# Performance work log

Hardware: AMD Instinct MI355X
Metric: run time of the kernel (lower is better)

## Reference

```python
import jax, jax.numpy as jnp
import numpy as np

N = 100000
E = 1200000


def _gcn_norm(edge_index, num_nodes):
    # Add self-loops and compute symmetric normalization (PyG GCNConv default).
    row = jnp.concatenate([edge_index[0], jnp.arange(num_nodes, dtype=edge_index.dtype)])
    col = jnp.concatenate([edge_index[1], jnp.arange(num_nodes, dtype=edge_index.dtype)])
    deg = jax.ops.segment_sum(jnp.ones_like(col, dtype=jnp.float32), col, num_segments=num_nodes)
    dinv = jnp.where(deg > 0, jax.lax.rsqrt(jnp.maximum(deg, 1.0)), 0.0)
    norm = dinv[row] * dinv[col]  # [E+N]
    return row, col, norm


def _gcn_conv(x, W, b, row, col, norm, num_nodes):
    h = x @ W                      # [N, out] dense transform first (fewer bytes to gather)
    msg = h[row] * norm[:, None]   # gather + edge-wise scale
    out = jax.ops.segment_sum(msg, col, num_segments=num_nodes)  # scatter-add to targets
    return out + b


def setup_inputs() -> dict:
    key = jax.random.key(0)
    k1, k2, k3, k4 = jax.random.split(key, 4)
    x = jax.random.normal(k1, (N, 128), dtype=jnp.float32)
    edge_index = jax.random.randint(k2, (2, E), 0, N, dtype=jnp.int64)
    W1 = jax.random.normal(k3, (128, 256), dtype=jnp.float32) * (1.0 / np.sqrt(128))
    b1 = jnp.zeros((256,), dtype=jnp.float32)
    W2 = jax.random.normal(k4, (256, 40), dtype=jnp.float32) * (1.0 / np.sqrt(256))
    b2 = jnp.zeros((40,), dtype=jnp.float32)
    return {"x": x, "edge_index": edge_index, "W1": W1, "b1": b1, "W2": W2, "b2": b2}


def reference(x, edge_index, W1, b1, W2, b2):
    row, col, norm = _gcn_norm(edge_index, N)
    h = _gcn_conv(x, W1, b1, row, col, norm, N)
    h = jax.nn.relu(h)
    # dropout omitted: eval mode (training=False) is identity
    return _gcn_conv(h, W2, b2, row, col, norm, N)
```

## Files before the change

### kernel.cpp

```cpp
#include <hip/hip_runtime.h>
#include <hip/hip_bf16.h>

#define NN 100000
#define EE 1200000
#define F1 128
#define F2 256
#define F3 40
#define MROWS 64
#define NBUK ((NN + 255) / 256)
#define NBLK 256
#define CHUNK ((EE + NBLK - 1) / NBLK)
#define DCAP 4096
#define XB2 ((NN * 32 + 255) / 256)
#define WB ((F1 * F2 + F2 * 48 + 255) / 256)

typedef __bf16 bf16x8 __attribute__((ext_vector_type(8)));
typedef float  f32x4  __attribute__((ext_vector_type(4)));

__device__ __forceinline__ unsigned short f2bf(float f) {
    unsigned u = __float_as_uint(f);
    return (unsigned short)((u + 0x7fffu + ((u >> 16) & 1u)) >> 16);
}
__device__ __forceinline__ float bflo(unsigned v) { return __uint_as_float(v << 16); }
__device__ __forceinline__ float bfhi(unsigned v) { return __uint_as_float(v & 0xffff0000u); }

__global__ __launch_bounds__(256) void k_scatprep(
    const int* __restrict__ row, const int* __restrict__ col,
    int* __restrict__ bcur, unsigned* __restrict__ rec,
    const float4* __restrict__ x, uint2* __restrict__ xh,
    const float* __restrict__ W1, const float* __restrict__ W2,
    __hip_bfloat16* __restrict__ W1p, __hip_bfloat16* __restrict__ W2p) {
    if (blockIdx.x < NBLK) {
        __shared__ int lh[NBUK];
        __shared__ int lbase[NBUK];
        for (int i = threadIdx.x; i < NBUK; i += 256) lh[i] = 0;
        __syncthreads();
        const int e0 = blockIdx.x * CHUNK;
        const int e1 = min(e0 + CHUNK, EE);
        for (int e = e0 + threadIdx.x; e < e1; e += 256) {
            int c = col[e];
            if ((unsigned)c < (unsigned)NN) atomicAdd(&lh[c >> 8], 1);
        }
        __syncthreads();
        for (int i = threadIdx.x; i < NBUK; i += 256) {
            int cn = lh[i];
            lbase[i] = cn ? atomicAdd(&bcur[i], cn) : 0;
            lh[i] = 0;
        }
        __syncthreads();
        for (int e = e0 + threadIdx.x; e < e1; e += 256) {
            int r = row[e], c = col[e];
            if ((unsigned)c < (unsigned)NN) {
                int b = c >> 8;
                int pos = lbase[b] + atomicAdd(&lh[b], 1);
                if (pos < DCAP)
                    rec[(size_t)b * DCAP + pos] =
                        ((unsigned)r & 0xFFFFFFu) | ((unsigned)(c & 255) << 24);
            }
        }
    } else if (blockIdx.x < NBLK + XB2) {
        int idx = (blockIdx.x - NBLK) * 256 + threadIdx.x;
        float4 v = x[idx];
        uint2 o;
        o.x = (unsigned)f2bf(v.x) | ((unsigned)f2bf(v.y) << 16);
        o.y = (unsigned)f2bf(v.z) | ((unsigned)f2bf(v.w) << 16);
        xh[idx] = o;
    } else {
        int idx = (blockIdx.x - NBLK - XB2) * 256 + threadIdx.x;
        if (idx < F1 * F2) {
            int k = idx / F2, c = idx - (idx / F2) * F2;
            int k8 = k >> 3, j = k & 7;
            W1p[((size_t)(k8 * F2 + c) << 3) + j] = __float2bfloat16(W1[(size_t)k * F2 + c]);
        } else {
            int i2 = idx - F1 * F2;
            int k = i2 / 48, c = i2 - (i2 / 48) * 48;
            int k8 = k >> 3, j = k & 7;
            float v = (c < F3) ? W2[(size_t)k * F3 + c] : 0.0f;
            W2p[((size_t)(k8 * 48 + c) << 3) + j] = __float2bfloat16(v);
        }
    }
}

__global__ __launch_bounds__(256) void k_csr(const int* __restrict__ bcur,
                                             const unsigned* __restrict__ rec,
                                             int* __restrict__ eidx,
                                             int* __restrict__ cnt,
                                             int* __restrict__ cursor,
                                             float* __restrict__ dinv) {
    __shared__ int lcnt[256];
    __shared__ int s[256];
    __shared__ int lcur[256];
    __shared__ unsigned lrec[DCAP];
    __shared__ int lde[DCAP];
    const int b = blockIdx.x;
    const int tid = threadIdx.x;
    lcnt[tid] = 0;
    __syncthreads();
    const int base = b * DCAP;
    const int nb = min(bcur[b], DCAP);
    for (int j = tid; j < nb; j += 256) {
        unsigned v = rec[(size_t)base + j];
        lrec[j] = v;
        atomicAdd(&lcnt[v >> 24], 1);
    }
    __syncthreads();
    int cv = lcnt[tid];
    s[tid] = cv;
    __syncthreads();
    int acc = cv;
    for (int d = 1; d < 256; d <<= 1) {
        int add = (tid >= d) ? s[tid - d] : 0;
        __syncthreads();
        acc += add;
        s[tid] = acc;
        __syncthreads();
    }
    int excl = acc - cv;
    lcur[tid] = excl;
    const int node = (b << 8) + tid;
    if (node < NN) {
        cnt[node] = cv;
        cursor[node] = base + excl + cv;
        dinv[node] = rsqrtf((float)(cv + 1));
    }
    __syncthreads();
    for (int j = tid; j < nb; j += 256) {
        unsigned v = lrec[j];
        int pos = atomicAdd(&lcur[v >> 24], 1);
        lde[pos] = (int)(v & 0xFFFFFFu);
    }
    __syncthreads();
    for (int j = tid; j < nb; j += 256) eidx[base + j] = lde[j];
}

__global__ __launch_bounds__(256) void k_agg1(const int* __restrict__ cursor,
                                              const int* __restrict__ cnt,
                                              const int* __restrict__ eidx,
                                              const float* __restrict__ dinv,
                                              const unsigned* __restrict__ xh,
                                              unsigned* __restrict__ agg) {
    int node = blockIdx.x * 4 + (threadIdx.x >> 6);
    int lane = threadIdx.x & 63;
    if (node >= NN) return;
    float dn = dinv[node];
    unsigned vs = xh[((size_t)node << 6) + lane];
    float a0 = bflo(vs) * dn, a1 = bfhi(vs) * dn;
    int n = cnt[node];
    int s = cursor[node] - n;
    int k = 0;
    for (; k + 7 < n; k += 8) {
        int r0 = eidx[s + k + 0], r1 = eidx[s + k + 1];
        int r2 = eidx[s + k + 2], r3 = eidx[s + k + 3];
        int r4 = eidx[s + k + 4], r5 = eidx[s + k + 5];
        int r6 = eidx[s + k + 6], r7 = eidx[s + k + 7];
        float d0 = dinv[r0], d1 = dinv[r1], d2 = dinv[r2], d3 = dinv[r3];
        float d4 = dinv[r4], d5 = dinv[r5], d6 = dinv[r6], d7 = dinv[r7];
        unsigned v0 = xh[((size_t)r0 << 6) + lane];
        unsigned v1 = xh[((size_t)r1 << 6) + lane];
        unsigned v2 = xh[((size_t)r2 << 6) + lane];
        unsigned v3 = xh[((size_t)r3 << 6) + lane];
        unsigned v4 = xh[((size_t)r4 << 6) + lane];
        unsigned v5 = xh[((size_t)r5 << 6) + lane];
        unsigned v6 = xh[((size_t)r6 << 6) + lane];
        unsigned v7 = xh[((size_t)r7 << 6) + lane];
        a0 += bflo(v0) * d0; a1 += bfhi(v0) * d0;
        a0 += bflo(v1) * d1; a1 += bfhi(v1) * d1;
        a0 += bflo(v2) * d2; a1 += bfhi(v2) * d2;
        a0 += bflo(v3) * d3; a1 += bfhi(v3) * d3;
        a0 += bflo(v4) * d4; a1 += bfhi(v4) * d4;
        a0 += bflo(v5) * d5; a1 += bfhi(v5) * d5;
        a0 += bflo(v6) * d6; a1 += bfhi(v6) * d6;
        a0 += bflo(v7) * d7; a1 += bfhi(v7) * d7;
    }
    for (; k + 3 < n; k += 4) {
        int r0 = eidx[s + k + 0], r1 = eidx[s + k + 1];
        int r2 = eidx[s + k + 2], r3 = eidx[s + k + 3];
        float d0 = dinv[r0], d1 = dinv[r1], d2 = dinv[r2], d3 = dinv[r3];
        unsigned v0 = xh[((size_t)r0 << 6) + lane];
        unsigned v1 = xh[((size_t)r1 << 6) + lane];
        unsigned v2 = xh[((size_t)r2 << 6) + lane];
        unsigned v3 = xh[((size_t)r3 << 6) + lane];
        a0 += bflo(v0) * d0; a1 += bfhi(v0) * d0;
        a0 += bflo(v1) * d1; a1 += bfhi(v1) * d1;
        a0 += bflo(v2) * d2; a1 += bfhi(v2) * d2;
        a0 += bflo(v3) * d3; a1 += bfhi(v3) * d3;
    }
    for (; k < n; ++k) {
        int r0 = eidx[s + k];
        float d0 = dinv[r0];
        unsigned v0 = xh[((size_t)r0 << 6) + lane];
        a0 += bflo(v0) * d0; a1 += bfhi(v0) * d0;
    }
    agg[((size_t)node << 6) + lane] = (unsigned)f2bf(a0 * dn) | ((unsigned)f2bf(a1 * dn) << 16);
}

__global__ __launch_bounds__(256) void k_gemm_mfma(
    const __hip_bfloat16* __restrict__ agg, const __hip_bfloat16* __restrict__ W1p,
    const float* __restrict__ b1, const __hip_bfloat16* __restrict__ W2p,
    const float* __restrict__ dinv, unsigned short* __restrict__ tg) {
    __shared__ __hip_bfloat16 h_s[MROWS][F2 + 8];
    const int i0   = blockIdx.x * MROWS;
    const int wave = threadIdx.x >> 6;
    const int lane = threadIdx.x & 63;
    const int m = lane & 15, q = lane >> 4;
    const int rowA = i0 + wave * 16 + m;

    f32x4 acc[16];
#pragma unroll
    for (int c = 0; c < 16; ++c) acc[c] = (f32x4){0.f, 0.f, 0.f, 0.f};

#pragma unroll
    for (int s = 0; s < 4; ++s) {
        bf16x8 a;
#pragma unroll
        for (int j = 0; j < 8; ++j) a[j] = (__bf16)0.0f;
        if (rowA < NN) a = *(const bf16x8*)(agg + (size_t)rowA * F1 + s * 32 + q * 8);
        const __hip_bfloat16* bp = W1p + ((size_t)(4 * s + q) * F2) * 8;
#pragma unroll
        for (int c = 0; c < 16; ++c) {
            bf16x8 b = *(const bf16x8*)(bp + ((size_t)(c * 16 + m) << 3));
            acc[c] = __builtin_amdgcn_mfma_f32_16x16x32_bf16(a, b, acc[c], 0, 0, 0);
        }
    }

#pragma unroll
    for (int c = 0; c < 16; ++c) {
        int col = c * 16 + m;
        float bj = b1[col];
#pragma unroll
        for (int r = 0; r < 4; ++r) {
            int lr = wave * 16 + q * 4 + r;
            h_s[lr][col] = __float2bfloat16(fmaxf(acc[c][r] + bj, 0.0f));
        }
    }
    __syncthreads();

    f32x4 acc2[3];
#pragma unroll
    for (int c = 0; c < 3; ++c) acc2[c] = (f32x4){0.f, 0.f, 0.f, 0.f};

#pragma unroll
    for (int s = 0; s < 8; ++s) {
        bf16x8 a = *(const bf16x8*)(&h_s[wave * 16 + m][s * 32 + q * 8]);
        const __hip_bfloat16* bp = W2p + ((size_t)(4 * s + q) * 48) * 8;
#pragma unroll
        for (int c = 0; c < 3; ++c) {
            bf16x8 b = *(const bf16x8*)(bp + ((size_t)(c * 16 + m) << 3));
            acc2[c] = __builtin_amdgcn_mfma_f32_16x16x32_bf16(a, b, acc2[c], 0, 0, 0);
        }
    }

#pragma unroll
    for (int c = 0; c < 3; ++c) {
        int col = c * 16 + m;
        if (col < F3) {
#pragma unroll
            for (int r = 0; r < 4; ++r) {
                int grow = i0 + wave * 16 + q * 4 + r;
                if (grow < NN)
                    tg[(size_t)grow * F3 + col] = f2bf(acc2[c][r] * dinv[grow]);
            }
        }
    }
}

__global__ __launch_bounds__(256) void k_agg2(const int* __restrict__ cursor,
                                              const int* __restrict__ cnt,
                                              const int* __restrict__ eidx,
                                              const float* __restrict__ dinv,
                                              const unsigned short* __restrict__ tg,
                                              const float* __restrict__ b2,
                                              float* __restrict__ out) {
    const int wave = threadIdx.x >> 6;
    const int lane = threadIdx.x & 63;
    const int g = lane / 10;
    const int t = lane - g * 10;
    const int node = blockIdx.x * 24 + wave * 6 + g;
    if (g >= 6 || node >= NN) return;
    const uint2* __restrict__ tg2 = (const uint2*)tg;

    uint2 v = tg2[(size_t)node * 10 + t];
    float a0 = bflo(v.x), a1 = bfhi(v.x), a2 = bflo(v.y), a3 = bfhi(v.y);
    const int n = cnt[node];
    const int s = cursor[node] - n;
    int k = 0;
    for (; k + 7 < n; k += 8) {
        int r0 = eidx[s + k + 0], r1 = eidx[s + k + 1];
        int r2 = eidx[s + k + 2], r3 = eidx[s + k + 3];
        int r4 = eidx[s + k + 4], r5 = eidx[s + k + 5];
        int r6 = eidx[s + k + 6], r7 = eidx[s + k + 7];
        uint2 v0 = tg2[(size_t)r0 * 10 + t];
        uint2 v1 = tg2[(size_t)r1 * 10 + t];
        uint2 v2 = tg2[(size_t)r2 * 10 + t];
        uint2 v3 = tg2[(size_t)r3 * 10 + t];
        uint2 v4 = tg2[(size_t)r4 * 10 + t];
        uint2 v5 = tg2[(size_t)r5 * 10 + t];
        uint2 v6 = tg2[(size_t)r6 * 10 + t];
        uint2 v7 = tg2[(size_t)r7 * 10 + t];
        a0 += bflo(v0.x); a1 += bfhi(v0.x); a2 += bflo(v0.y); a3 += bfhi(v0.y);
        a0 += bflo(v1.x); a1 += bfhi(v1.x); a2 += bflo(v1.y); a3 += bfhi(v1.y);
        a0 += bflo(v2.x); a1 += bfhi(v2.x); a2 += bflo(v2.y); a3 += bfhi(v2.y);
        a0 += bflo(v3.x); a1 += bfhi(v3.x); a2 += bflo(v3.y); a3 += bfhi(v3.y);
        a0 += bflo(v4.x); a1 += bfhi(v4.x); a2 += bflo(v4.y); a3 += bfhi(v4.y);
        a0 += bflo(v5.x); a1 += bfhi(v5.x); a2 += bflo(v5.y); a3 += bfhi(v5.y);
        a0 += bflo(v6.x); a1 += bfhi(v6.x); a2 += bflo(v6.y); a3 += bfhi(v6.y);
        a0 += bflo(v7.x); a1 += bfhi(v7.x); a2 += bflo(v7.y); a3 += bfhi(v7.y);
    }
    for (; k + 3 < n; k += 4) {
        int r0 = eidx[s + k + 0], r1 = eidx[s + k + 1];
        int r2 = eidx[s + k + 2], r3 = eidx[s + k + 3];
        uint2 v0 = tg2[(size_t)r0 * 10 + t];
        uint2 v1 = tg2[(size_t)r1 * 10 + t];
        uint2 v2 = tg2[(size_t)r2 * 10 + t];
        uint2 v3 = tg2[(size_t)r3 * 10 + t];
        a0 += bflo(v0.x); a1 += bfhi(v0.x); a2 += bflo(v0.y); a3 += bfhi(v0.y);
        a0 += bflo(v1.x); a1 += bfhi(v1.x); a2 += bflo(v1.y); a3 += bfhi(v1.y);
        a0 += bflo(v2.x); a1 += bfhi(v2.x); a2 += bflo(v2.y); a3 += bfhi(v2.y);
        a0 += bflo(v3.x); a1 += bfhi(v3.x); a2 += bflo(v3.y); a3 += bfhi(v3.y);
    }
    for (; k < n; ++k) {
        uint2 v0 = tg2[(size_t)eidx[s + k] * 10 + t];
        a0 += bflo(v0.x); a1 += bfhi(v0.x); a2 += bflo(v0.y); a3 += bfhi(v0.y);
    }
    float d = dinv[node];
    float4 bb = *(const float4*)(b2 + 4 * t);
    float4 o;
    o.x = a0 * d + bb.x;
    o.y = a1 * d + bb.y;
    o.z = a2 * d + bb.z;
    o.w = a3 * d + bb.w;
    *(float4*)(out + (size_t)node * F3 + 4 * t) = o;
}

extern "C" void kernel_launch(void* const* d_in, const int* in_sizes, int n_in,
                              void* d_out, int out_size, void* d_ws, size_t ws_size,
                              hipStream_t stream) {
    const float* x  = (const float*)d_in[0];
    const int*   ei = (const int*)d_in[1];
    const float* W1 = (const float*)d_in[2];
    const float* b1 = (const float*)d_in[3];
    const float* W2 = (const float*)d_in[4];
    const float* b2 = (const float*)d_in[5];
    float* out = (float*)d_out;

    const int* row = ei;
    const int* col = ei + EE;

    int* cnt     = (int*)d_ws;
    int* cursor  = cnt + NN;
    float* dinv  = (float*)(cursor + NN);
    int* bcur    = (int*)(dinv + NN);
    int* eidx    = bcur + NBUK + 9;
    unsigned* xh  = (unsigned*)(eidx + NBUK * DCAP);
    unsigned* agg = xh + (size_t)NN * 64;
    unsigned* rec = agg;
    unsigned short* tg = (unsigned short*)xh;
    __hip_bfloat16* W1p = (__hip_bfloat16*)(agg + (size_t)NN * 64);
    __hip_bfloat16* W2p = W1p + (size_t)F1 * F2;

    hipMemsetAsync(bcur, 0, NBUK * sizeof(int), stream);
    k_scatprep<<<NBLK + XB2 + WB, 256, 0, stream>>>(
        row, col, bcur, rec, (const float4*)x, (uint2*)xh, W1, W2, W1p, W2p);
    k_csr<<<NBUK, 256, 0, stream>>>(bcur, rec, eidx, cnt, cursor, dinv);

    k_agg1<<<(NN + 3) / 4, 256, 0, stream>>>(cursor, cnt, eidx, dinv, xh, agg);
    k_gemm_mfma<<<(NN + MROWS - 1) / MROWS, 256, 0, stream>>>(
        (const __hip_bfloat16*)agg, W1p, b1, W2p, dinv, tg);
    k_agg2<<<(NN + 23) / 24, 256, 0, stream>>>(cursor, cnt, eidx, dinv, tg, b2, out);
}
```

Baseline: 266.2 us.

## Slice bf16 features into 8 column planes so aggregation gathers stay cache-local

The bf16 copy of x is stored as 8 column slices of 16 features each (32 bytes per node per slice). Layer-1 aggregation then runs one block per (node group, slice), with 8 edges handled in parallel per wave and a shuffle reduction at the end. The GEMM reads its A operand from the same sliced layout. The aim is to keep each slice's gather working set (about 3.2 MB) small enough to hit in cache. The cost is 8x as many aggregation blocks, each reading eidx and dinv again, plus shorter 32-byte gather segments.

```diff
diff --git a/kernel.cpp b/kernel.cpp
--- a/kernel.cpp
+++ b/kernel.cpp
@@ -11,7 +11,7 @@
 #define NBLK 256
 #define CHUNK ((EE + NBLK - 1) / NBLK)
 #define DCAP 4096
-#define XB2 ((NN * 32 + 255) / 256)
+#define XP8 (NN * 8 / 256)
 #define WB ((F1 * F2 + F2 * 48 + 255) / 256)
 
 typedef __bf16 bf16x8 __attribute__((ext_vector_type(8)));
@@ -27,7 +27,7 @@
 __global__ __launch_bounds__(256) void k_scatprep(
     const int* __restrict__ row, const int* __restrict__ col,
     int* __restrict__ bcur, unsigned* __restrict__ rec,
-    const float4* __restrict__ x, uint2* __restrict__ xh,
+    const float4* __restrict__ x, unsigned* __restrict__ xhs,
     const float* __restrict__ W1, const float* __restrict__ W2,
     __hip_bfloat16* __restrict__ W1p, __hip_bfloat16* __restrict__ W2p) {
     if (blockIdx.x < NBLK) {
@@ -58,15 +58,24 @@
                         ((unsigned)r & 0xFFFFFFu) | ((unsigned)(c & 255) << 24);
             }
         }
-    } else if (blockIdx.x < NBLK + XB2) {
+    } else if (blockIdx.x < NBLK + XP8) {
         int idx = (blockIdx.x - NBLK) * 256 + threadIdx.x;
-        float4 v = x[idx];
-        uint2 o;
-        o.x = (unsigned)f2bf(v.x) | ((unsigned)f2bf(v.y) << 16);
-        o.y = (unsigned)f2bf(v.z) | ((unsigned)f2bf(v.w) << 16);
-        xh[idx] = o;
+        int node = idx >> 3, s = idx & 7;
+        const float4* xp = x + (size_t)node * 32 + s * 4;
+        float4 v0 = xp[0], v1 = xp[1], v2 = xp[2], v3 = xp[3];
+        uint4 o0, o1;
+        o0.x = (unsigned)f2bf(v0.x) | ((unsigned)f2bf(v0.y) << 16);
+        o0.y = (unsigned)f2bf(v0.z) | ((unsigned)f2bf(v0.w) << 16);
+        o0.z = (unsigned)f2bf(v1.x) | ((unsigned)f2bf(v1.y) << 16);
+        o0.w = (unsigned)f2bf(v1.z) | ((unsigned)f2bf(v1.w) << 16);
+        o1.x = (unsigned)f2bf(v2.x) | ((unsigned)f2bf(v2.y) << 16);
+        o1.y = (unsigned)f2bf(v2.z) | ((unsigned)f2bf(v2.w) << 16);
+        o1.z = (unsigned)f2bf(v3.x) | ((unsigned)f2bf(v3.y) << 16);
+        o1.w = (unsigned)f2bf(v3.z) | ((unsigned)f2bf(v3.w) << 16);
+        uint4* dst = (uint4*)(xhs + ((size_t)s * NN + node) * 8);
+        dst[0] = o0; dst[1] = o1;
     } else {
-        int idx = (blockIdx.x - NBLK - XB2) * 256 + threadIdx.x;
+        int idx = (blockIdx.x - NBLK - XP8) * 256 + threadIdx.x;
         if (idx < F1 * F2) {
             int k = idx / F2, c = idx - (idx / F2) * F2;
             int k8 = k >> 3, j = k & 7;
@@ -137,65 +146,51 @@
                                               const int* __restrict__ cnt,
                                               const int* __restrict__ eidx,
                                               const float* __restrict__ dinv,
-                                              const unsigned* __restrict__ xh,
-                                              unsigned* __restrict__ agg) {
-    int node = blockIdx.x * 4 + (threadIdx.x >> 6);
-    int lane = threadIdx.x & 63;
-    if (node >= NN) return;
-    float dn = dinv[node];
-    unsigned vs = xh[((size_t)node << 6) + lane];
-    float a0 = bflo(vs) * dn, a1 = bfhi(vs) * dn;
-    int n = cnt[node];
-    int s = cursor[node] - n;
-    int k = 0;
-    for (; k + 7 < n; k += 8) {
-        int r0 = eidx[s + k + 0], r1 = eidx[s + k + 1];
-        int r2 = eidx[s + k + 2], r3 = eidx[s + k + 3];
-        int r4 = eidx[s + k + 4], r5 = eidx[s + k + 5];
-        int r6 = eidx[s + k + 6], r7 = eidx[s + k + 7];
-        float d0 = dinv[r0], d1 = dinv[r1], d2 = dinv[r2], d3 = dinv[r3];
-        float d4 = dinv[r4], d5 = dinv[r5], d6 = dinv[r6], d7 = dinv[r7];
-        unsigned v0 = xh[((size_t)r0 << 6) + lane];
-        unsigned v1 = xh[((size_t)r1 << 6) + lane];
-        unsigned v2 = xh[((size_t)r2 << 6) + lane];
-        unsigned v3 = xh[((size_t)r3 << 6) + lane];
-        unsigned v4 = xh[((size_t)r4 << 6) + lane];
-        unsigned v5 = xh[((size_t)r5 << 6) + lane];
-        unsigned v6 = xh[((size_t)r6 << 6) + lane];
-        unsigned v7 = xh[((size_t)r7 << 6) + lane];
+                                              const unsigned* __restrict__ xhs,
+                                              unsigned* __restrict__ aggs) {
+    const int s = blockIdx.x & 7;
+    const int g = blockIdx.x >> 3;
+    const int wave = threadIdx.x >> 6;
+    const int lane = threadIdx.x & 63;
+    const int e = lane >> 3, d = lane & 7;
+    const int node = g * 4 + wave;
+    const unsigned* __restrict__ xs = xhs + (size_t)s * (NN * 8);
+    const float dn = dinv[node];
+    float a0 = 0.f, a1 = 0.f;
+    if (e == 0) {
+        unsigned vs = xs[(size_t)node * 8 + d];
+        a0 = bflo(vs) * dn; a1 = bfhi(vs) * dn;
+    }
+    const int n = cnt[node];
+    const int st = cursor[node] - n;
+    int k = e;
+    for (; k + 8 < n; k += 16) {
+        int r0 = eidx[st + k];
+        int r1 = eidx[st + k + 8];
+        float d0 = dinv[r0], d1 = dinv[r1];
+        unsigned v0 = xs[(size_t)r0 * 8 + d];
+        unsigned v1 = xs[(size_t)r1 * 8 + d];
         a0 += bflo(v0) * d0; a1 += bfhi(v0) * d0;
         a0 += bflo(v1) * d1; a1 += bfhi(v1) * d1;
-        a0 += bflo(v2) * d2; a1 += bfhi(v2) * d2;
-        a0 += bflo(v3) * d3; a1 += bfhi(v3) * d3;
-        a0 += bflo(v4) * d4; a1 += bfhi(v4) * d4;
-        a0 += bflo(v5) * d5; a1 += bfhi(v5) * d5;
-        a0 += bflo(v6) * d6; a1 += bfhi(v6) * d6;
-        a0 += bflo(v7) * d7; a1 += bfhi(v7) * d7;
-    }
-    for (; k + 3 < n; k += 4) {
-        int r0 = eidx[s + k + 0], r1 = eidx[s + k + 1];
-        int r2 = eidx[s + k + 2], r3 = eidx[s + k + 3];
-        float d0 = dinv[r0], d1 = dinv[r1], d2 = dinv[r2], d3 = dinv[r3];
-        unsigned v0 = xh[((size_t)r0 << 6) + lane];
-        unsigned v1 = xh[((size_t)r1 << 6) + lane];
-        unsigned v2 = xh[((size_t)r2 << 6) + lane];
-        unsigned v3 = xh[((size_t)r3 << 6) + lane];
+    }
+    if (k < n) {
+        int r0 = eidx[st + k];
+        float d0 = dinv[r0];
+        unsigned v0 = xs[(size_t)r0 * 8 + d];
         a0 += bflo(v0) * d0; a1 += bfhi(v0) * d0;
-        a0 += bflo(v1) * d1; a1 += bfhi(v1) * d1;
-        a0 += bflo(v2) * d2; a1 += bfhi(v2) * d2;
-        a0 += bflo(v3) * d3; a1 += bfhi(v3) * d3;
-    }
-    for (; k < n; ++k) {
-        int r0 = eidx[s + k];
-        float d0 = dinv[r0];
-        unsigned v0 = xh[((size_t)r0 << 6) + lane];
-        a0 += bflo(v0) * d0; a1 += bfhi(v0) * d0;
-    }
-    agg[((size_t)node << 6) + lane] = (unsigned)f2bf(a0 * dn) | ((unsigned)f2bf(a1 * dn) << 16);
+    }
+#pragma unroll
+    for (int off = 8; off < 64; off <<= 1) {
+        a0 += __shfl_xor(a0, off);
+        a1 += __shfl_xor(a1, off);
+    }
+    if (e == 0)
+        aggs[((size_t)s * NN + node) * 8 + d] =
+            (unsigned)f2bf(a0 * dn) | ((unsigned)f2bf(a1 * dn) << 16);
 }
 
 __global__ __launch_bounds__(256) void k_gemm_mfma(
-    const __hip_bfloat16* __restrict__ agg, const __hip_bfloat16* __restrict__ W1p,
+    const unsigned* __restrict__ aggs, const __hip_bfloat16* __restrict__ W1p,
     const float* __restrict__ b1, const __hip_bfloat16* __restrict__ W2p,
     const float* __restrict__ dinv, unsigned short* __restrict__ tg) {
     __shared__ __hip_bfloat16 h_s[MROWS][F2 + 8];
@@ -214,7 +209,11 @@
         bf16x8 a;
 #pragma unroll
         for (int j = 0; j < 8; ++j) a[j] = (__bf16)0.0f;
-        if (rowA < NN) a = *(const bf16x8*)(agg + (size_t)rowA * F1 + s * 32 + q * 8);
+        if (rowA < NN) {
+            const uint4* ap = (const uint4*)(aggs +
+                ((size_t)(2 * s + (q >> 1)) * NN + rowA) * 8 + (q & 1) * 4);
+            a = __builtin_bit_cast(bf16x8, *ap);
+        }
         const __hip_bfloat16* bp = W1p + ((size_t)(4 * s + q) * F2) * 8;
 #pragma unroll
         for (int c = 0; c < 16; ++c) {
@@ -351,20 +350,20 @@
     float* dinv  = (float*)(cursor + NN);
     int* bcur    = (int*)(dinv + NN);
     int* eidx    = bcur + NBUK + 9;
-    unsigned* xh  = (unsigned*)(eidx + NBUK * DCAP);
-    unsigned* agg = xh + (size_t)NN * 64;
-    unsigned* rec = agg;
-    unsigned short* tg = (unsigned short*)xh;
-    __hip_bfloat16* W1p = (__hip_bfloat16*)(agg + (size_t)NN * 64);
+    unsigned* xhs  = (unsigned*)(eidx + NBUK * DCAP);
+    unsigned* aggs = xhs + (size_t)NN * 64;
+    unsigned* rec = aggs;
+    unsigned short* tg = (unsigned short*)xhs;
+    __hip_bfloat16* W1p = (__hip_bfloat16*)(aggs + (size_t)NN * 64);
     __hip_bfloat16* W2p = W1p + (size_t)F1 * F2;
 
     hipMemsetAsync(bcur, 0, NBUK * sizeof(int), stream);
-    k_scatprep<<<NBLK + XB2 + WB, 256, 0, stream>>>(
-        row, col, bcur, rec, (const float4*)x, (uint2*)xh, W1, W2, W1p, W2p);
+    k_scatprep<<<NBLK + XP8 + WB, 256, 0, stream>>>(
+        row, col, bcur, rec, (const float4*)x, xhs, W1, W2, W1p, W2p);
     k_csr<<<NBUK, 256, 0, stream>>>(bcur, rec, eidx, cnt, cursor, dinv);
 
-    k_agg1<<<(NN + 3) / 4, 256, 0, stream>>>(cursor, cnt, eidx, dinv, xh, agg);
+    k_agg1<<<(NN / 4) * 8, 256, 0, stream>>>(cursor, cnt, eidx, dinv, xhs, aggs);
     k_gemm_mfma<<<(NN + MROWS - 1) / MROWS, 256, 0, stream>>>(
-        (const __hip_bfloat16*)agg, W1p, b1, W2p, dinv, tg);
+        aggs, W1p, b1, W2p, dinv, tg);
     k_agg2<<<(NN + 23) / 24, 256, 0, stream>>>(cursor, cnt, eidx, dinv, tg, b2, out);
 }
```

New measurement: 419.5 us. +57.6%, slower.
